# Optimization experiments

Hardware: AMD Instinct MI355X
Metric: run time of the kernel (lower is better)

The kernel has to match this reference:

```python
import jax, jax.numpy as jnp
import numpy as np

N_DENSE = 13
N_SPARSE = 26
SPARSE_DIM = 100                       # all sparse vocab sizes equal
N_FIELD = N_DENSE + N_SPARSE           # 39
N_FEATURES = N_DENSE + N_SPARSE * SPARSE_DIM  # 2613
K = 16
BATCH = 16384


def setup_inputs() -> dict:
    key = jax.random.key(0)
    k1, k2, k3, k4, k5 = jax.random.split(key, 5)
    dense = jax.random.normal(k1, (BATCH, N_DENSE), dtype=jnp.float32)
    sparse = jax.random.randint(k2, (BATCH, N_SPARSE), 0, SPARSE_DIM).astype(jnp.float32)
    x = jnp.concatenate([dense, sparse], axis=1)  # [B, 39]
    # nn.Linear(n_features, 1) params
    lim = 1.0 / np.sqrt(N_FEATURES)
    w_weight = jax.random.uniform(k3, (1, N_FEATURES), jnp.float32, -lim, lim)
    w_bias = jax.random.uniform(k4, (1,), jnp.float32, -lim, lim)
    # v initialized to zeros in the module; use small randn so grads are nontrivial
    v = jax.random.normal(k5, (N_FEATURES, N_FIELD, K), dtype=jnp.float32) * 0.01
    return {"x": x, "w_weight": w_weight, "w_bias": w_bias, "v": v}


def _build_inputs(x):
    dense_x = x[:, :N_DENSE]                             # [B, 13]
    sparse_x = x[:, N_DENSE:].astype(jnp.int32)          # [B, 26]
    oh = jax.nn.one_hot(sparse_x, SPARSE_DIM, dtype=jnp.float32)  # [B, 26, 100]
    return jnp.concatenate([dense_x, oh.reshape(x.shape[0], -1)], axis=1)  # [B, 2613]


def reference(x, w_weight, w_bias, v):
    inputs = _build_inputs(x)                            # [B, n_features]
    linear_part = inputs @ w_weight.T + w_bias           # [B, 1]
    field_f = jnp.einsum('bn,nfk->bfk', inputs, v)       # [B, n_field, k]
    # sum_{i<j} <f_i, f_j> = 0.5 * ((sum_f)^2 - sum_f f^2), summed over k
    s = jnp.sum(field_f, axis=1)                         # [B, k]
    sq = jnp.sum(field_f * field_f, axis=1)              # [B, k]
    cross_part = 0.5 * jnp.sum(s * s - sq, axis=1, keepdims=True)  # [B, 1]
    return jax.nn.sigmoid(linear_part + cross_part)
```

## Files before the change

kernel.cpp:

```cpp
#include <hip/hip_runtime.h>
#include <hip/hip_fp16.h>
#include <math.h>

#define N_DENSE 13
#define N_SPARSE 26
#define SPARSE_DIM 100
#define N_FIELD 39
#define N_FIELD_P 40
#define KDIM 16
#define N_FEATURES 2613
#define ROW_F 624
#define ROW_DW 320
#define THREADS 256
#define ROWS_PER_BLOCK 4

__global__ __launch_bounds__(ROW_DW) void cvt_pad_f16(
    const float* __restrict__ v, __half2* __restrict__ o)
{
    int n = blockIdx.x;
    int d = threadIdx.x;
    __half2 r = __floats2half2_rn(0.f, 0.f);
    if (d < ROW_F / 2) {
        float2 f = *reinterpret_cast<const float2*>(v + (size_t)n * ROW_F + 2 * d);
        r = __floats2half2_rn(f.x, f.y);
    }
    o[(size_t)n * ROW_DW + d] = r;
}

__global__ __launch_bounds__(THREADS, 8) void ffm_f16(
    const float* __restrict__ x,
    const float* __restrict__ w,
    const float* __restrict__ bias,
    const __half2* __restrict__ vb,
    float* __restrict__ out,
    int B)
{
    __shared__ __half2 ldsDense[N_DENSE * ROW_DW];
    {
        const uint4* src = reinterpret_cast<const uint4*>(vb);
        uint4* dst = reinterpret_cast<uint4*>(ldsDense);
        for (int i = threadIdx.x; i < N_DENSE * ROW_DW / 4; i += THREADS)
            dst[i] = src[i];
    }
    __syncthreads();

    const int l = threadIdx.x & 63;
    const int wv = __builtin_amdgcn_readfirstlane((int)(threadIdx.x >> 6));
    const int row = blockIdx.x * ROWS_PER_BLOCK + wv;
    if (row >= B) return;

    const float* xr = x + row * (N_DENSE + N_SPARSE);

    __half2 acc[5];
#pragma unroll
    for (int m = 0; m < 5; ++m) acc[m] = __floats2half2_rn(0.f, 0.f);

    float lin = bias[0];

#pragma unroll
    for (int j = 0; j < N_DENSE; ++j) {
        float xv = xr[j];
        lin = fmaf(xv, w[j], lin);
        __half2 xh = __float2half2_rn(xv);
#pragma unroll
        for (int m = 0; m < 5; ++m)
            acc[m] = __hfma2(xh, ldsDense[j * ROW_DW + 64 * m + l], acc[m]);
    }

#pragma unroll
    for (int s = 0; s < N_SPARSE; s += 2) {
        int i0 = N_DENSE + s * SPARSE_DIM + (int)xr[N_DENSE + s];
        int i1 = N_DENSE + (s + 1) * SPARSE_DIM + (int)xr[N_DENSE + s + 1];
        const __half2* b0 = vb + (size_t)i0 * ROW_DW + l;
        const __half2* b1 = vb + (size_t)i1 * ROW_DW + l;
        __half2 u0 = b0[0],   v0 = b1[0];
        __half2 u1 = b0[64],  v1 = b1[64];
        __half2 u2 = b0[128], v2 = b1[128];
        __half2 u3 = b0[192], v3 = b1[192];
        __half2 u4 = b0[256], v4 = b1[256];
        lin += w[i0] + w[i1];
        acc[0] = __hadd2(acc[0], u0); acc[0] = __hadd2(acc[0], v0);
        acc[1] = __hadd2(acc[1], u1); acc[1] = __hadd2(acc[1], v1);
        acc[2] = __hadd2(acc[2], u2); acc[2] = __hadd2(acc[2], v2);
        acc[3] = __hadd2(acc[3], u3); acc[3] = __hadd2(acc[3], v3);
        acc[4] = __hadd2(acc[4], u4); acc[4] = __hadd2(acc[4], v4);
    }

    float sx = 0.f, sy = 0.f, qx = 0.f, qy = 0.f;
#pragma unroll
    for (int m = 0; m < 5; ++m) {
        float ax = __low2float(acc[m]);
        float ay = __high2float(acc[m]);
        sx += ax; sy += ay;
        qx = fmaf(ax, ax, qx);
        qy = fmaf(ay, ay, qy);
    }
#pragma unroll
    for (int mask = 8; mask <= 32; mask <<= 1) {
        sx += __shfl_xor(sx, mask);
        sy += __shfl_xor(sy, mask);
        qx += __shfl_xor(qx, mask);
        qy += __shfl_xor(qy, mask);
    }
    float c = (sx * sx - qx) + (sy * sy - qy);
    c += __shfl_xor(c, 1);
    c += __shfl_xor(c, 2);
    c += __shfl_xor(c, 4);

    float logit = lin + 0.5f * c;
    if (l == 0) out[row] = 1.f / (1.f + expf(-logit));
}

#define ROW_Q (ROW_F / 4)
__global__ __launch_bounds__(256) void ffm_fp32(
    const float* __restrict__ x, const float* __restrict__ w,
    const float* __restrict__ bias, const float* __restrict__ v,
    float* __restrict__ out, int B)
{
    __shared__ float ldsDense[N_DENSE * ROW_F];
    const float4* v4 = reinterpret_cast<const float4*>(v);
    float4* lds4 = reinterpret_cast<float4*>(ldsDense);
    for (int i = threadIdx.x; i < N_DENSE * ROW_Q; i += 256) lds4[i] = v4[i];
    __syncthreads();

    const int g = threadIdx.x >> 4, l = threadIdx.x & 15;
    const int row = blockIdx.x * 16 + g;
    if (row >= B) return;
    const float* xr = x + row * (N_DENSE + N_SPARSE);

    float4 acc[10];
#pragma unroll
    for (int i = 0; i < 10; ++i) acc[i] = make_float4(0.f, 0.f, 0.f, 0.f);
#pragma unroll
    for (int j = 0; j < N_DENSE; ++j) {
        float xv = xr[j];
        const float4* b = lds4 + j * ROW_Q;
#pragma unroll
        for (int i = 0; i < 10; ++i)
            if (i < 9 || l < 12) {
                float4 t = b[l + 16 * i];
                acc[i].x += xv * t.x; acc[i].y += xv * t.y;
                acc[i].z += xv * t.z; acc[i].w += xv * t.w;
            }
    }
    int nidx[N_SPARSE];
#pragma unroll
    for (int s = 0; s < N_SPARSE; ++s)
        nidx[s] = N_DENSE + s * SPARSE_DIM + (int)xr[N_DENSE + s];
    for (int s = 0; s < N_SPARSE; ++s) {
        const float4* b = v4 + (size_t)nidx[s] * ROW_Q;
#pragma unroll
        for (int i = 0; i < 10; ++i)
            if (i < 9 || l < 12) {
                float4 t = b[l + 16 * i];
                acc[i].x += t.x; acc[i].y += t.y; acc[i].z += t.z; acc[i].w += t.w;
            }
    }
    float4 s4 = make_float4(0,0,0,0), q4 = make_float4(0,0,0,0);
#pragma unroll
    for (int i = 0; i < 10; ++i) {
        s4.x += acc[i].x; s4.y += acc[i].y; s4.z += acc[i].z; s4.w += acc[i].w;
        q4.x += acc[i].x*acc[i].x; q4.y += acc[i].y*acc[i].y;
        q4.z += acc[i].z*acc[i].z; q4.w += acc[i].w*acc[i].w;
    }
#pragma unroll
    for (int m = 4; m <= 8; m <<= 1) {
        s4.x += __shfl_xor(s4.x,m); s4.y += __shfl_xor(s4.y,m);
        s4.z += __shfl_xor(s4.z,m); s4.w += __shfl_xor(s4.w,m);
        q4.x += __shfl_xor(q4.x,m); q4.y += __shfl_xor(q4.y,m);
        q4.z += __shfl_xor(q4.z,m); q4.w += __shfl_xor(q4.w,m);
    }
    float c = (s4.x*s4.x - q4.x) + (s4.y*s4.y - q4.y) +
              (s4.z*s4.z - q4.z) + (s4.w*s4.w - q4.w);
    c += __shfl_xor(c,1); c += __shfl_xor(c,2);
    float lin = bias[0];
#pragma unroll
    for (int j = 0; j < N_DENSE; ++j) lin += xr[j]*w[j];
#pragma unroll
    for (int s = 0; s < N_SPARSE; ++s) lin += w[nidx[s]];
    float logit = lin + 0.5f*c;
    if (l == 0) out[row] = 1.f/(1.f+expf(-logit));
}

extern "C" void kernel_launch(void* const* d_in, const int* in_sizes, int n_in,
                              void* d_out, int out_size, void* d_ws, size_t ws_size,
                              hipStream_t stream) {
    const float* x    = (const float*)d_in[0];
    const float* w    = (const float*)d_in[1];
    const float* bias = (const float*)d_in[2];
    const float* v    = (const float*)d_in[3];
    float* out = (float*)d_out;

    int B = in_sizes[0] / (N_DENSE + N_SPARSE);
    size_t need = (size_t)N_FEATURES * ROW_DW * sizeof(__half2);

    if (ws_size >= need) {
        cvt_pad_f16<<<N_FEATURES, ROW_DW, 0, stream>>>(v, (__half2*)d_ws);
        int grid = (B + ROWS_PER_BLOCK - 1) / ROWS_PER_BLOCK;
        ffm_f16<<<grid, THREADS, 0, stream>>>(x, w, bias, (const __half2*)d_ws, out, B);
    } else {
        int grid = (B + 15) / 16;
        ffm_fp32<<<grid, 256, 0, stream>>>(x, w, bias, v, out, B);
    }
}
```

Measured before the change: 39.20 us.

## Use persistent grid-stride blocks and lane-parallel linear term in FFM kernel

```diff
diff --git a/kernel.cpp b/kernel.cpp
--- a/kernel.cpp
+++ b/kernel.cpp
@@ -13,6 +13,7 @@
 #define ROW_DW 320
 #define THREADS 256
 #define ROWS_PER_BLOCK 4
+#define GRID_BLOCKS 2048
 
 __global__ __launch_bounds__(ROW_DW) void cvt_pad_f16(
     const float* __restrict__ v, __half2* __restrict__ o)
@@ -27,7 +28,7 @@
     o[(size_t)n * ROW_DW + d] = r;
 }
 
-__global__ __launch_bounds__(THREADS, 8) void ffm_f16(
+__global__ __launch_bounds__(THREADS, 8) void ffm_f16s(
     const float* __restrict__ x,
     const float* __restrict__ w,
     const float* __restrict__ bias,
@@ -46,69 +47,72 @@
 
     const int l = threadIdx.x & 63;
     const int wv = __builtin_amdgcn_readfirstlane((int)(threadIdx.x >> 6));
-    const int row = blockIdx.x * ROWS_PER_BLOCK + wv;
-    if (row >= B) return;
-
-    const float* xr = x + row * (N_DENSE + N_SPARSE);
-
-    __half2 acc[5];
-#pragma unroll
-    for (int m = 0; m < 5; ++m) acc[m] = __floats2half2_rn(0.f, 0.f);
-
-    float lin = bias[0];
-
-#pragma unroll
-    for (int j = 0; j < N_DENSE; ++j) {
-        float xv = xr[j];
-        lin = fmaf(xv, w[j], lin);
-        __half2 xh = __float2half2_rn(xv);
-#pragma unroll
-        for (int m = 0; m < 5; ++m)
-            acc[m] = __hfma2(xh, ldsDense[j * ROW_DW + 64 * m + l], acc[m]);
-    }
-
-#pragma unroll
-    for (int s = 0; s < N_SPARSE; s += 2) {
-        int i0 = N_DENSE + s * SPARSE_DIM + (int)xr[N_DENSE + s];
-        int i1 = N_DENSE + (s + 1) * SPARSE_DIM + (int)xr[N_DENSE + s + 1];
-        const __half2* b0 = vb + (size_t)i0 * ROW_DW + l;
-        const __half2* b1 = vb + (size_t)i1 * ROW_DW + l;
-        __half2 u0 = b0[0],   v0 = b1[0];
-        __half2 u1 = b0[64],  v1 = b1[64];
-        __half2 u2 = b0[128], v2 = b1[128];
-        __half2 u3 = b0[192], v3 = b1[192];
-        __half2 u4 = b0[256], v4 = b1[256];
-        lin += w[i0] + w[i1];
-        acc[0] = __hadd2(acc[0], u0); acc[0] = __hadd2(acc[0], v0);
-        acc[1] = __hadd2(acc[1], u1); acc[1] = __hadd2(acc[1], v1);
-        acc[2] = __hadd2(acc[2], u2); acc[2] = __hadd2(acc[2], v2);
-        acc[3] = __hadd2(acc[3], u3); acc[3] = __hadd2(acc[3], v3);
-        acc[4] = __hadd2(acc[4], u4); acc[4] = __hadd2(acc[4], v4);
-    }
-
-    float sx = 0.f, sy = 0.f, qx = 0.f, qy = 0.f;
-#pragma unroll
-    for (int m = 0; m < 5; ++m) {
-        float ax = __low2float(acc[m]);
-        float ay = __high2float(acc[m]);
-        sx += ax; sy += ay;
-        qx = fmaf(ax, ax, qx);
-        qy = fmaf(ay, ay, qy);
-    }
-#pragma unroll
-    for (int mask = 8; mask <= 32; mask <<= 1) {
-        sx += __shfl_xor(sx, mask);
-        sy += __shfl_xor(sy, mask);
-        qx += __shfl_xor(qx, mask);
-        qy += __shfl_xor(qy, mask);
-    }
-    float c = (sx * sx - qx) + (sy * sy - qy);
-    c += __shfl_xor(c, 1);
-    c += __shfl_xor(c, 2);
-    c += __shfl_xor(c, 4);
-
-    float logit = lin + 0.5f * c;
-    if (l == 0) out[row] = 1.f / (1.f + expf(-logit));
+    const float b0 = bias[0];
+
+    for (int row = blockIdx.x * ROWS_PER_BLOCK + wv; row < B;
+         row += GRID_BLOCKS * ROWS_PER_BLOCK) {
+
+        const float* xr = x + (size_t)row * N_FIELD;
+
+        float xv_l = 0.f;
+        if (l < N_FIELD) xv_l = xr[l];
+        float linp = 0.f;
+        if (l < N_DENSE) {
+            linp = xv_l * w[l];
+        } else if (l < N_FIELD) {
+            int idx = N_DENSE + (l - N_DENSE) * SPARSE_DIM + (int)xv_l;
+            linp = w[idx];
+        }
+
+        __half2 acc[5];
+#pragma unroll
+        for (int m = 0; m < 5; ++m) acc[m] = __floats2half2_rn(0.f, 0.f);
+
+#pragma unroll
+        for (int j = 0; j < N_DENSE; ++j) {
+            __half2 xh = __float2half2_rn(xr[j]);
+#pragma unroll
+            for (int m = 0; m < 5; ++m)
+                acc[m] = __hfma2(xh, ldsDense[j * ROW_DW + 64 * m + l], acc[m]);
+        }
+
+#pragma unroll
+        for (int s = 0; s < N_SPARSE; ++s) {
+            int su = __builtin_amdgcn_readfirstlane((int)xr[N_DENSE + s]);
+            const __half2* b =
+                vb + (size_t)(N_DENSE + s * SPARSE_DIM + su) * ROW_DW + l;
+            acc[0] = __hadd2(acc[0], b[0]);
+            acc[1] = __hadd2(acc[1], b[64]);
+            acc[2] = __hadd2(acc[2], b[128]);
+            acc[3] = __hadd2(acc[3], b[192]);
+            acc[4] = __hadd2(acc[4], b[256]);
+        }
+
+        float sx = 0.f, sy = 0.f, qx = 0.f, qy = 0.f;
+#pragma unroll
+        for (int m = 0; m < 5; ++m) {
+            float ax = __low2float(acc[m]);
+            float ay = __high2float(acc[m]);
+            sx += ax; sy += ay;
+            qx = fmaf(ax, ax, qx);
+            qy = fmaf(ay, ay, qy);
+        }
+#pragma unroll
+        for (int mask = 8; mask <= 32; mask <<= 1) {
+            sx   += __shfl_xor(sx, mask);
+            sy   += __shfl_xor(sy, mask);
+            qx   += __shfl_xor(qx, mask);
+            qy   += __shfl_xor(qy, mask);
+            linp += __shfl_xor(linp, mask);
+        }
+        float u = 0.5f * ((sx * sx - qx) + (sy * sy - qy)) + linp;
+        u += __shfl_xor(u, 1);
+        u += __shfl_xor(u, 2);
+        u += __shfl_xor(u, 4);
+
+        float logit = b0 + u;
+        if (l == 0) out[row] = 1.f / (1.f + expf(-logit));
+    }
 }
 
 #define ROW_Q (ROW_F / 4)
@@ -196,8 +200,8 @@
 
     if (ws_size >= need) {
         cvt_pad_f16<<<N_FEATURES, ROW_DW, 0, stream>>>(v, (__half2*)d_ws);
-        int grid = (B + ROWS_PER_BLOCK - 1) / ROWS_PER_BLOCK;
-        ffm_f16<<<grid, THREADS, 0, stream>>>(x, w, bias, (const __half2*)d_ws, out, B);
+        ffm_f16s<<<GRID_BLOCKS, THREADS, 0, stream>>>(
+            x, w, bias, (const __half2*)d_ws, out, B);
     } else {
         int grid = (B + 15) / 16;
         ffm_fp32<<<grid, 256, 0, stream>>>(x, w, bias, v, out, B);
```

Measured after the change: 104.3 us. 166% more time.

## Load row via lane-parallel x read, shuffle-broadcast indices, and wider 8-byte gathers

Applied to the files above, without the earlier changes.

```diff
diff --git a/kernel.cpp b/kernel.cpp
--- a/kernel.cpp
+++ b/kernel.cpp
@@ -6,11 +6,11 @@
 #define N_SPARSE 26
 #define SPARSE_DIM 100
 #define N_FIELD 39
-#define N_FIELD_P 40
 #define KDIM 16
 #define N_FEATURES 2613
 #define ROW_F 624
 #define ROW_DW 320
+#define ROW_BYTES 1280
 #define THREADS 256
 #define ROWS_PER_BLOCK 4
 
@@ -27,7 +27,11 @@
     o[(size_t)n * ROW_DW + d] = r;
 }
 
-__global__ __launch_bounds__(THREADS, 8) void ffm_f16(
+__device__ __forceinline__ __half2 h2(unsigned int v) {
+    return *reinterpret_cast<__half2*>(&v);
+}
+
+__global__ __launch_bounds__(THREADS, 8) void ffm_v7(
     const float* __restrict__ x,
     const float* __restrict__ w,
     const float* __restrict__ bias,
@@ -45,69 +49,101 @@
     __syncthreads();
 
     const int l = threadIdx.x & 63;
-    const int wv = __builtin_amdgcn_readfirstlane((int)(threadIdx.x >> 6));
-    const int row = blockIdx.x * ROWS_PER_BLOCK + wv;
+    const int p = l & 3;
+    const int t = l >> 2;
+    const int u = t & 1;
+    const int row = blockIdx.x * ROWS_PER_BLOCK + (threadIdx.x >> 6);
     if (row >= B) return;
 
-    const float* xr = x + row * (N_DENSE + N_SPARSE);
-
-    __half2 acc[5];
-#pragma unroll
-    for (int m = 0; m < 5; ++m) acc[m] = __floats2half2_rn(0.f, 0.f);
-
-    float lin = bias[0];
+    const float b0v = bias[0];
+
+    float xv = 0.f;
+    if (l < N_FIELD) xv = x[(size_t)row * N_FIELD + l];
+    int idx = 0;
+    if (l >= N_DENSE && l < N_FIELD)
+        idx = N_DENSE + (l - N_DENSE) * SPARSE_DIM + (int)xv;
+
+    float linp = 0.f;
+    if (l < N_FIELD) {
+        float wv = w[l < N_DENSE ? l : idx];
+        linp = (l < N_DENSE) ? xv * wv : wv;
+    }
+
+    const int o1 = 8 * l;
+    const int o2 = 512 + 8 * l;
+    const int oB = 1024 + ((t >> 1) << 5) + (p << 3) + (u << 2);
+    const int dB = oB >> 2;
+
+    __half2 zero = __floats2half2_rn(0.f, 0.f);
+    __half2 aP0 = zero, aP1 = zero, aQ0 = zero, aQ1 = zero, aB = zero;
 
 #pragma unroll
     for (int j = 0; j < N_DENSE; ++j) {
-        float xv = xr[j];
-        lin = fmaf(xv, w[j], lin);
-        __half2 xh = __float2half2_rn(xv);
-#pragma unroll
-        for (int m = 0; m < 5; ++m)
-            acc[m] = __hfma2(xh, ldsDense[j * ROW_DW + 64 * m + l], acc[m]);
+        float xj = __shfl(xv, j);
+        __half2 xh = __float2half2_rn(xj);
+        const uint2* b64 = reinterpret_cast<const uint2*>(ldsDense + j * ROW_DW);
+        uint2 d1 = b64[l];
+        uint2 d2 = b64[64 + l];
+        unsigned int dB32 =
+            reinterpret_cast<const unsigned int*>(ldsDense + j * ROW_DW)[dB];
+        aP0 = __hfma2(xh, h2(d1.x), aP0);
+        aP1 = __hfma2(xh, h2(d1.y), aP1);
+        aQ0 = __hfma2(xh, h2(d2.x), aQ0);
+        aQ1 = __hfma2(xh, h2(d2.y), aQ1);
+        aB  = __hfma2(xh, h2(dB32), aB);
     }
 
 #pragma unroll
     for (int s = 0; s < N_SPARSE; s += 2) {
-        int i0 = N_DENSE + s * SPARSE_DIM + (int)xr[N_DENSE + s];
-        int i1 = N_DENSE + (s + 1) * SPARSE_DIM + (int)xr[N_DENSE + s + 1];
-        const __half2* b0 = vb + (size_t)i0 * ROW_DW + l;
-        const __half2* b1 = vb + (size_t)i1 * ROW_DW + l;
-        __half2 u0 = b0[0],   v0 = b1[0];
-        __half2 u1 = b0[64],  v1 = b1[64];
-        __half2 u2 = b0[128], v2 = b1[128];
-        __half2 u3 = b0[192], v3 = b1[192];
-        __half2 u4 = b0[256], v4 = b1[256];
-        lin += w[i0] + w[i1];
-        acc[0] = __hadd2(acc[0], u0); acc[0] = __hadd2(acc[0], v0);
-        acc[1] = __hadd2(acc[1], u1); acc[1] = __hadd2(acc[1], v1);
-        acc[2] = __hadd2(acc[2], u2); acc[2] = __hadd2(acc[2], v2);
-        acc[3] = __hadd2(acc[3], u3); acc[3] = __hadd2(acc[3], v3);
-        acc[4] = __hadd2(acc[4], u4); acc[4] = __hadd2(acc[4], v4);
-    }
-
-    float sx = 0.f, sy = 0.f, qx = 0.f, qy = 0.f;
-#pragma unroll
-    for (int m = 0; m < 5; ++m) {
-        float ax = __low2float(acc[m]);
-        float ay = __high2float(acc[m]);
-        sx += ax; sy += ay;
-        qx = fmaf(ax, ax, qx);
-        qy = fmaf(ay, ay, qy);
-    }
-#pragma unroll
-    for (int mask = 8; mask <= 32; mask <<= 1) {
-        sx += __shfl_xor(sx, mask);
-        sy += __shfl_xor(sy, mask);
-        qx += __shfl_xor(qx, mask);
-        qy += __shfl_xor(qy, mask);
-    }
-    float c = (sx * sx - qx) + (sy * sy - qy);
-    c += __shfl_xor(c, 1);
-    c += __shfl_xor(c, 2);
-    c += __shfl_xor(c, 4);
-
-    float logit = lin + 0.5f * c;
+        int i0 = __shfl(idx, N_DENSE + s);
+        int i1 = __shfl(idx, N_DENSE + s + 1);
+        const char* r0 = reinterpret_cast<const char*>(vb) + (size_t)i0 * ROW_BYTES;
+        const char* r1 = reinterpret_cast<const char*>(vb) + (size_t)i1 * ROW_BYTES;
+        uint2 a0 = *reinterpret_cast<const uint2*>(r0 + o1);
+        uint2 c0 = *reinterpret_cast<const uint2*>(r0 + o2);
+        unsigned int e0 = *reinterpret_cast<const unsigned int*>(r0 + oB);
+        uint2 a1 = *reinterpret_cast<const uint2*>(r1 + o1);
+        uint2 c1 = *reinterpret_cast<const uint2*>(r1 + o2);
+        unsigned int e1 = *reinterpret_cast<const unsigned int*>(r1 + oB);
+        aP0 = __hadd2(aP0, h2(a0.x)); aP1 = __hadd2(aP1, h2(a0.y));
+        aQ0 = __hadd2(aQ0, h2(c0.x)); aQ1 = __hadd2(aQ1, h2(c0.y));
+        aB  = __hadd2(aB,  h2(e0));
+        aP0 = __hadd2(aP0, h2(a1.x)); aP1 = __hadd2(aP1, h2(a1.y));
+        aQ0 = __hadd2(aQ0, h2(c1.x)); aQ1 = __hadd2(aQ1, h2(c1.y));
+        aB  = __hadd2(aB,  h2(e1));
+    }
+
+    float fP[4] = { __low2float(aP0), __high2float(aP0),
+                    __low2float(aP1), __high2float(aP1) };
+    float fQ[4] = { __low2float(aQ0), __high2float(aQ0),
+                    __low2float(aQ1), __high2float(aQ1) };
+    float bb0 = __low2float(aB), bb1 = __high2float(aB);
+    float e0 = u ? 0.f : bb0, e1 = u ? 0.f : bb1;
+    float e2 = u ? bb0 : 0.f, e3 = u ? bb1 : 0.f;
+
+    float s0 = fP[0] + fQ[0] + e0;
+    float s1 = fP[1] + fQ[1] + e1;
+    float s2 = fP[2] + fQ[2] + e2;
+    float s3 = fP[3] + fQ[3] + e3;
+    float q0 = fP[0]*fP[0] + fQ[0]*fQ[0] + e0*e0;
+    float q1 = fP[1]*fP[1] + fQ[1]*fQ[1] + e1*e1;
+    float q2 = fP[2]*fP[2] + fQ[2]*fQ[2] + e2*e2;
+    float q3 = fP[3]*fP[3] + fQ[3]*fQ[3] + e3*e3;
+
+#pragma unroll
+    for (int m = 4; m <= 32; m <<= 1) {
+        s0 += __shfl_xor(s0, m); s1 += __shfl_xor(s1, m);
+        s2 += __shfl_xor(s2, m); s3 += __shfl_xor(s3, m);
+        q0 += __shfl_xor(q0, m); q1 += __shfl_xor(q1, m);
+        q2 += __shfl_xor(q2, m); q3 += __shfl_xor(q3, m);
+        linp += __shfl_xor(linp, m);
+    }
+    float cpart = (s0*s0 - q0) + (s1*s1 - q1) + (s2*s2 - q2) + (s3*s3 - q3);
+    float uval = 0.5f * cpart + linp;
+    uval += __shfl_xor(uval, 1);
+    uval += __shfl_xor(uval, 2);
+
+    float logit = b0v + uval;
     if (l == 0) out[row] = 1.f / (1.f + expf(-logit));
 }
 
@@ -138,9 +174,9 @@
 #pragma unroll
         for (int i = 0; i < 10; ++i)
             if (i < 9 || l < 12) {
-                float4 t = b[l + 16 * i];
-                acc[i].x += xv * t.x; acc[i].y += xv * t.y;
-                acc[i].z += xv * t.z; acc[i].w += xv * t.w;
+                float4 tt = b[l + 16 * i];
+                acc[i].x += xv * tt.x; acc[i].y += xv * tt.y;
+                acc[i].z += xv * tt.z; acc[i].w += xv * tt.w;
             }
     }
     int nidx[N_SPARSE];
@@ -152,8 +188,8 @@
 #pragma unroll
         for (int i = 0; i < 10; ++i)
             if (i < 9 || l < 12) {
-                float4 t = b[l + 16 * i];
-                acc[i].x += t.x; acc[i].y += t.y; acc[i].z += t.z; acc[i].w += t.w;
+                float4 tt = b[l + 16 * i];
+                acc[i].x += tt.x; acc[i].y += tt.y; acc[i].z += tt.z; acc[i].w += tt.w;
             }
     }
     float4 s4 = make_float4(0,0,0,0), q4 = make_float4(0,0,0,0);
@@ -197,7 +233,8 @@
     if (ws_size >= need) {
         cvt_pad_f16<<<N_FEATURES, ROW_DW, 0, stream>>>(v, (__half2*)d_ws);
         int grid = (B + ROWS_PER_BLOCK - 1) / ROWS_PER_BLOCK;
-        ffm_f16<<<grid, THREADS, 0, stream>>>(x, w, bias, (const __half2*)d_ws, out, B);
+        ffm_v7<<<grid, THREADS, 0, stream>>>(
+            x, w, bias, (const __half2*)d_ws, out, B);
     } else {
         int grid = (B + 15) / 16;
         ffm_fp32<<<grid, 256, 0, stream>>>(x, w, bias, v, out, B);
```

Result: slower. 53.48 us (+36.4%).
